# Kernel tuning notes

Measured on AMD Instinct MI355X. Metric: run time of the kernel, lower is better.

## Reference

```python
import jax, jax.numpy as jnp
import numpy as np

# Mistral-7B attention dims
B, S, D = 4, 1024, 4096
NH, NKV, HD = 32, 8, 128
SLIDING_WINDOW = 4096


def setup_inputs() -> dict:
    key = jax.random.key(0)
    ks = jax.random.split(key, 6)
    x = jax.random.normal(ks[0], (B, S, D), jnp.float32) * 0.02
    wq = jax.random.normal(ks[1], (NH * HD, D), jnp.float32) * 0.02
    wk = jax.random.normal(ks[2], (NKV * HD, D), jnp.float32) * 0.02
    wv = jax.random.normal(ks[3], (NKV * HD, D), jnp.float32) * 0.02
    wo = jax.random.normal(ks[4], (D, NH * HD), jnp.float32) * 0.02
    # RoPE frequencies (theta=10000), shape [S, HD//2]
    inv_freq = 1.0 / (10000.0 ** (jnp.arange(0, HD, 2, dtype=jnp.float32) / HD))
    angles = jnp.arange(S, dtype=jnp.float32)[:, None] * inv_freq[None, :]
    freqs_cos = jnp.cos(angles)
    freqs_sin = jnp.sin(angles)
    # sliding-window causal additive mask [S, S]
    i = jnp.arange(S)
    visible = (i[:, None] >= i[None, :]) & (i[:, None] - i[None, :] < SLIDING_WINDOW)
    mask = jnp.where(visible, 0.0, -1e9).astype(jnp.float32)
    positions = jnp.arange(S, dtype=jnp.int32)
    return {
        'x': x, 'wq': wq, 'wk': wk, 'wv': wv, 'wo': wo,
        'freqs_cos': freqs_cos, 'freqs_sin': freqs_sin,
        'mask': mask, 'positions': positions, 'seqlen': S,
    }


def _rope(t, fc, fs):
    # t: [B, S, H, HD]; fc/fs: [S, HD//2]; interleaved real/imag complex rotation
    tr = t[..., 0::2]
    ti = t[..., 1::2]
    fc = fc[None, :, None, :]
    fs = fs[None, :, None, :]
    out_r = tr * fc - ti * fs
    out_i = tr * fs + ti * fc
    return jnp.stack([out_r, out_i], axis=-1).reshape(t.shape)


def reference(x, wq, wk, wv, wo, freqs_cos, freqs_sin, mask, positions, seqlen):
    bsz = x.shape[0]
    scale = HD ** -0.5
    # QKV projections (TtLinear: y = x @ W^T, no bias)
    q = (x @ wq.T).reshape(bsz, seqlen, NH, HD)
    k = (x @ wk.T).reshape(bsz, seqlen, NKV, HD)
    v = (x @ wv.T).reshape(bsz, seqlen, NKV, HD)
    # inline rotary embedding on q, k
    q = _rope(q, freqs_cos, freqs_sin)
    k = _rope(k, freqs_cos, freqs_sin)
    # GQA: repeat_interleave kv heads (prefill path: positions.shape[0] > 1)
    rep = NH // NKV
    k = jnp.repeat(k, rep, axis=2)  # [B, S, NH, HD]
    v = jnp.repeat(v, rep, axis=2)
    scores = jnp.einsum('bqhd,bkhd->bhqk', q, k) * scale + mask[None, None]
    attn = jax.nn.softmax(scores, axis=-1)
    out = jnp.einsum('bhqk,bkhd->bqhd', attn, v).reshape(bsz, seqlen, NH * HD)
    return out @ wo.T
```

## Files before the change

kernel.cpp:

```cpp
#include <hip/hip_runtime.h>
#include <hip/hip_bf16.h>
#include <stdint.h>


typedef __bf16 bf16x8 __attribute__((ext_vector_type(8)));
typedef float floatx4 __attribute__((ext_vector_type(4)));

__device__ __forceinline__ unsigned short f2bf(float f) {
    union { float f; uint32_t u; } v; v.f = f;
    uint32_t u = v.u;
    uint32_t r = (u + 0x7FFFu + ((u >> 16) & 1u)) >> 16;
    return (unsigned short)r;
}
__device__ __forceinline__ float bf2f(unsigned short h) {
    union { uint32_t u; float f; } v; v.u = ((uint32_t)h) << 16;
    return v.f;
}

__device__ __forceinline__ void async_copy16(const void* g, void* l) {
    __builtin_amdgcn_global_load_lds(
        (const __attribute__((address_space(1))) unsigned int*)g,
        (__attribute__((address_space(3))) unsigned int*)l,
        16, 0, 0);
}

__global__ void cast_bf16_kernel(const float* __restrict__ in,
                                 unsigned short* __restrict__ out, int n4) {
    int i = blockIdx.x * blockDim.x + threadIdx.x;
    if (i >= n4) return;
    float4 v = ((const float4*)in)[i];
    ushort4 o;
    o.x = f2bf(v.x); o.y = f2bf(v.y); o.z = f2bf(v.z); o.w = f2bf(v.w);
    ((ushort4*)out)[i] = o;
}

#define GBM 128
#define GBN 128
#define GBK 64

__global__ __launch_bounds__(256)
void gemm_bt_kernel(const unsigned short* __restrict__ A,
                    const unsigned short* __restrict__ B,
                    void* __restrict__ Cout, int M, int N, int K, int out_is_bf16)
{
    __shared__ unsigned short As[GBM * GBK];
    __shared__ unsigned short Bs[GBN * GBK];

    const int tid  = threadIdx.x;
    const int lane = tid & 63;
    const int wave = tid >> 6;
    const int quad = lane >> 4;
    const int l15  = lane & 15;

    const int bm = blockIdx.y * GBM;
    const int bn = blockIdx.x * GBN;
    const int waveM = (wave >> 1) * 64;
    const int waveN = (wave & 1) * 64;

    floatx4 acc[4][4];
    #pragma unroll
    for (int i = 0; i < 4; i++)
        #pragma unroll
        for (int j = 0; j < 4; j++)
            acc[i][j] = floatx4{0.f, 0.f, 0.f, 0.f};

    const int srow = wave * 8 + (lane >> 3);
    const int gcol = (((lane & 7) ^ (lane >> 3)) << 4);
    uint8_t* AsB = (uint8_t*)As;
    uint8_t* BsB = (uint8_t*)Bs;

    for (int k0 = 0; k0 < K; k0 += GBK) {
        __syncthreads();
        const uint8_t* Ab = (const uint8_t*)A + (size_t)k0 * 2;
        const uint8_t* Bb = (const uint8_t*)B + (size_t)k0 * 2;
        #pragma unroll
        for (int i = 0; i < 4; i++) {
            int row = i * 32 + srow;
            async_copy16(Ab + (size_t)(bm + row) * K * 2 + gcol, AsB + i * 4096 + wave * 1024);
            async_copy16(Bb + (size_t)(bn + row) * K * 2 + gcol, BsB + i * 4096 + wave * 1024);
        }
        __syncthreads();

        #pragma unroll
        for (int kk = 0; kk < 2; kk++) {
            bf16x8 af[4], bfr[4];
            #pragma unroll
            for (int i = 0; i < 4; i++) {
                int row = waveM + i * 16 + l15;
                af[i] = *(const bf16x8*)(AsB + row * 128 +
                          ((((kk << 2) | quad) ^ (l15 & 7)) << 4));
            }
            #pragma unroll
            for (int j = 0; j < 4; j++) {
                int row = waveN + j * 16 + l15;
                bfr[j] = *(const bf16x8*)(BsB + row * 128 +
                          ((((kk << 2) | quad) ^ (l15 & 7)) << 4));
            }
            #pragma unroll
            for (int i = 0; i < 4; i++)
                #pragma unroll
                for (int j = 0; j < 4; j++)
                    acc[i][j] = __builtin_amdgcn_mfma_f32_16x16x32_bf16(af[i], bfr[j], acc[i][j], 0, 0, 0);
        }
    }

    const int rowBase = bm + waveM + quad * 4;
    const int colBase = bn + waveN + l15;
    if (out_is_bf16) {
        unsigned short* C = (unsigned short*)Cout;
        #pragma unroll
        for (int i = 0; i < 4; i++)
            #pragma unroll
            for (int j = 0; j < 4; j++)
                #pragma unroll
                for (int r = 0; r < 4; r++)
                    C[(size_t)(rowBase + i * 16 + r) * N + colBase + j * 16] = f2bf(acc[i][j][r]);
    } else {
        float* C = (float*)Cout;
        #pragma unroll
        for (int i = 0; i < 4; i++)
            #pragma unroll
            for (int j = 0; j < 4; j++)
                #pragma unroll
                for (int r = 0; r < 4; r++)
                    C[(size_t)(rowBase + i * 16 + r) * N + colBase + j * 16] = acc[i][j][r];
    }
}

__global__ __launch_bounds__(512, 2)
void gemm_bt_256_kernel(const unsigned short* __restrict__ A,
                        const unsigned short* __restrict__ B,
                        void* __restrict__ Cout, int M, int N, int K, int out_is_bf16)
{
    __shared__ uint8_t lds[4 * 32768];

    const int tid  = threadIdx.x;
    const int lane = tid & 63;
    const int wave = tid >> 6;
    const int quad = lane >> 4;
    const int l15  = lane & 15;
    const int wr   = wave >> 2;
    const int wc   = wave & 3;

    const int nwg = gridDim.x * gridDim.y;
    int orig = blockIdx.y * gridDim.x + blockIdx.x;
    int swzb = (nwg & 7) ? orig : ((orig & 7) * (nwg >> 3) + (orig >> 3));
    const int bm = (swzb / gridDim.x) * 256;
    const int bn = (swzb % gridDim.x) * 256;

    const int srow = wave * 32 + (lane >> 2);
    const int sg   = (((lane & 3) ^ ((lane >> 3) & 3)) << 4);
    const uint8_t* Ar0 = (const uint8_t*)(A + (size_t)(bm + srow) * K) + sg;
    const uint8_t* Ar1 = (const uint8_t*)(A + (size_t)(bm + srow + 16) * K) + sg;
    const uint8_t* Br0 = (const uint8_t*)(B + (size_t)(bn + srow) * K) + sg;
    const uint8_t* Br1 = (const uint8_t*)(B + (size_t)(bn + srow + 16) * K) + sg;
    const int ldsA0 = wave * 2048;
    const int ldsA1 = wave * 2048 + 1024;

    const int rsw  = (quad ^ ((l15 >> 1) & 3)) << 4;
    const int aoff = (wr * 128 + l15) * 64 + rsw;
    const int boff = 16384 + (wc * 64 + l15) * 64 + rsw;

    floatx4 acc[8][4];
    #pragma unroll
    for (int m = 0; m < 8; m++)
        #pragma unroll
        for (int n = 0; n < 4; n++)
            acc[m][n] = floatx4{0.f, 0.f, 0.f, 0.f};

    auto stage = [&](int t) {
        uint8_t* buf = lds + (size_t)(t & 3) * 32768;
        const size_t koff = (size_t)t * 64;
        async_copy16(Ar0 + koff, buf + ldsA0);
        async_copy16(Ar1 + koff, buf + ldsA1);
        async_copy16(Br0 + koff, buf + 16384 + ldsA0);
        async_copy16(Br1 + koff, buf + 16384 + ldsA1);
    };

    stage(0); stage(1); stage(2);

    const int NT = K >> 5;
    for (int t = 0; t < NT; ++t) {
        if (t < NT - 2)
            asm volatile("s_waitcnt vmcnt(8)\n\ts_barrier" ::: "memory");
        else if (t == NT - 2)
            asm volatile("s_waitcnt vmcnt(4)\n\ts_barrier" ::: "memory");
        else
            asm volatile("s_waitcnt vmcnt(0)\n\ts_barrier" ::: "memory");

        if (t + 3 < NT) stage(t + 3);

        const uint8_t* buf = lds + (size_t)(t & 3) * 32768;
        bf16x8 a0[4], b0[4], a1[4];
        #pragma unroll
        for (int m = 0; m < 4; m++) a0[m] = *(const bf16x8*)(buf + aoff + m * 1024);
        #pragma unroll
        for (int n = 0; n < 4; n++) b0[n] = *(const bf16x8*)(buf + boff + n * 1024);
        __builtin_amdgcn_s_setprio(1);
        #pragma unroll
        for (int m = 0; m < 4; m++)
            #pragma unroll
            for (int n = 0; n < 4; n++)
                acc[m][n] = __builtin_amdgcn_mfma_f32_16x16x32_bf16(a0[m], b0[n], acc[m][n], 0, 0, 0);
        __builtin_amdgcn_s_setprio(0);
        #pragma unroll
        for (int m = 0; m < 4; m++) a1[m] = *(const bf16x8*)(buf + aoff + (4 + m) * 1024);
        __builtin_amdgcn_s_setprio(1);
        #pragma unroll
        for (int m = 0; m < 4; m++)
            #pragma unroll
            for (int n = 0; n < 4; n++)
                acc[4 + m][n] = __builtin_amdgcn_mfma_f32_16x16x32_bf16(a1[m], b0[n], acc[4 + m][n], 0, 0, 0);
        __builtin_amdgcn_s_setprio(0);
    }

    const int rowBase = bm + wr * 128 + quad * 4;
    const int colBase = bn + wc * 64 + l15;
    if (out_is_bf16) {
        unsigned short* C = (unsigned short*)Cout;
        #pragma unroll
        for (int m = 0; m < 8; m++)
            #pragma unroll
            for (int n = 0; n < 4; n++)
                #pragma unroll
                for (int r = 0; r < 4; r++)
                    C[(size_t)(rowBase + m * 16 + r) * N + colBase + n * 16] = f2bf(acc[m][n][r]);
    } else {
        float* C = (float*)Cout;
        #pragma unroll
        for (int m = 0; m < 8; m++)
            #pragma unroll
            for (int n = 0; n < 4; n++)
                #pragma unroll
                for (int r = 0; r < 4; r++)
                    C[(size_t)(rowBase + m * 16 + r) * N + colBase + n * 16] = acc[m][n][r];
    }
}

__global__ void rope_kernel(unsigned short* __restrict__ t,
                            const float* __restrict__ fc,
                            const float* __restrict__ fs,
                            int nh, int total_pairs) {
    int idx = blockIdx.x * blockDim.x + threadIdx.x;
    if (idx >= total_pairs) return;
    int j   = idx & 63;
    int tmp = idx >> 6;
    int s   = (tmp / nh) & 1023;
    float c  = fc[s * 64 + j];
    float sn = fs[s * 64 + j];
    size_t base = (size_t)tmp * 128 + j * 2;
    float tr = bf2f(t[base]), ti = bf2f(t[base + 1]);
    t[base]     = f2bf(tr * c - ti * sn);
    t[base + 1] = f2bf(tr * sn + ti * c);
}

#define AS_  1024
#define AHD 128
#define ANH 32
#define ANKV 8

__global__ __launch_bounds__(256)
void attn_kernel(const unsigned short* __restrict__ Q,
                 const unsigned short* __restrict__ Kk,
                 const unsigned short* __restrict__ Vt,
                 unsigned short* __restrict__ O)
{
    __shared__ unsigned short Ks[64 * 136];
    __shared__ unsigned short Vs[128 * 72];
    __shared__ unsigned short Ps[4][16 * 72];

    const int tid  = threadIdx.x;
    const int lane = tid & 63;
    const int wave = tid >> 6;
    const int quad = lane >> 4;
    const int l15  = lane & 15;

    const int bid = blockIdx.x;
    const int qt = 15 - (bid & 15);
    const int h  = (bid >> 4) & 31;
    const int b  = bid >> 9;
    const int hk = h >> 2;
    const int q0 = qt * 64;

    bf16x8 aq[4];
    {
        const int qrow = q0 + wave * 16 + l15;
        const unsigned short* src = Q + ((size_t)((b * AS_ + qrow) * ANH + h)) * AHD;
        #pragma unroll
        for (int kk = 0; kk < 4; kk++)
            aq[kk] = *(const bf16x8*)(src + kk * 32 + quad * 8);
    }

    float lsum[4];
    #pragma unroll
    for (int r = 0; r < 4; r++) lsum[r] = 0.0f;
    floatx4 o[8];
    #pragma unroll
    for (int d = 0; d < 8; d++) o[d] = floatx4{0.f, 0.f, 0.f, 0.f};

    const float scale = 0.08838834764831845f;

    for (int kt = 0; kt <= qt; kt++) {
        __syncthreads();
        #pragma unroll
        for (int i = 0; i < 4; i++) {
            int c = tid + i * 256;
            int r = c >> 4, col = (c & 15) * 8;
            size_t krow = ((size_t)((b * AS_ + kt * 64 + r) * ANKV + hk)) * AHD;
            *(uint4*)(Ks + r * 136 + col) = *(const uint4*)(Kk + krow + col);
        }
        #pragma unroll
        for (int i = 0; i < 4; i++) {
            int c = tid + i * 256;
            int d = c >> 3, kk0 = (c & 7) * 8;
            const unsigned short* src =
                Vt + (size_t)(hk * AHD + d) * (4 * AS_) + b * AS_ + kt * 64 + kk0;
            *(uint4*)(Vs + d * 72 + kk0) = *(const uint4*)src;
        }
        __syncthreads();

        floatx4 sc[4];
        #pragma unroll
        for (int j = 0; j < 4; j++) {
            sc[j] = floatx4{0.f, 0.f, 0.f, 0.f};
            #pragma unroll
            for (int kk = 0; kk < 4; kk++) {
                bf16x8 bk = *(const bf16x8*)(Ks + (j * 16 + l15) * 136 + kk * 32 + quad * 8);
                sc[j] = __builtin_amdgcn_mfma_f32_16x16x32_bf16(aq[kk], bk, sc[j], 0, 0, 0);
            }
        }

        const bool diag = (kt == qt);
        #pragma unroll
        for (int r = 0; r < 4; r++) {
            const int qrow = q0 + wave * 16 + quad * 4 + r;
            float acc = 0.0f;
            #pragma unroll
            for (int j = 0; j < 4; j++) {
                float e = __expf(sc[j][r] * scale);
                if (diag) {
                    int key = kt * 64 + j * 16 + l15;
                    if (key > qrow) e = 0.0f;
                }
                acc += e;
                Ps[wave][(quad * 4 + r) * 72 + j * 16 + l15] = f2bf(e);
            }
            lsum[r] += acc;
        }

        #pragma unroll
        for (int kk = 0; kk < 2; kk++) {
            bf16x8 ap = *(const bf16x8*)(Ps[wave] + l15 * 72 + kk * 32 + quad * 8);
            #pragma unroll
            for (int d = 0; d < 8; d++) {
                bf16x8 bv = *(const bf16x8*)(Vs + (d * 16 + l15) * 72 + kk * 32 + quad * 8);
                o[d] = __builtin_amdgcn_mfma_f32_16x16x32_bf16(ap, bv, o[d], 0, 0, 0);
            }
        }
    }

    #pragma unroll
    for (int r = 0; r < 4; r++) {
        float s = lsum[r];
        #pragma unroll
        for (int off = 1; off < 16; off <<= 1)
            s += __shfl_xor(s, off, 64);
        float inv = 1.0f / s;
        int qrow = q0 + wave * 16 + quad * 4 + r;
        unsigned short* dst = O + ((size_t)((b * AS_ + qrow) * ANH + h)) * AHD;
        #pragma unroll
        for (int d = 0; d < 8; d++)
            dst[d * 16 + l15] = f2bf(o[d][r] * inv);
    }
}

extern "C" void kernel_launch(void* const* d_in, const int* in_sizes, int n_in,
                              void* d_out, int out_size, void* d_ws, size_t ws_size,
                              hipStream_t stream)
{
    const float* x  = (const float*)d_in[0];
    const float* wq = (const float*)d_in[1];
    const float* wk = (const float*)d_in[2];
    const float* wv = (const float*)d_in[3];
    const float* wo = (const float*)d_in[4];
    const float* fc = (const float*)d_in[5];
    const float* fs = (const float*)d_in[6];

    const int B = 4, S = 1024, D = 4096, NH = 32, NKV = 8, HD = 128;
    const int M    = B * S;
    const int NQ   = NH * HD;
    const int NKVD = NKV * HD;

    unsigned short* ws = (unsigned short*)d_ws;
    size_t off = 0;
    unsigned short* xb  = ws + off; off += (size_t)M * D;
    unsigned short* wqb = ws + off; off += (size_t)NQ * D;
    unsigned short* wkb = ws + off; off += (size_t)NKVD * D;
    unsigned short* wvb = ws + off; off += (size_t)NKVD * D;
    unsigned short* wob = ws + off; off += (size_t)D * NQ;
    unsigned short* qb  = ws + off; off += (size_t)M * NQ;
    unsigned short* kb  = ws + off; off += (size_t)M * NKVD;
    unsigned short* vtb = ws + off; off += (size_t)NKVD * M;
    unsigned short* aob = ws + off; off += (size_t)M * NQ;

    {
        struct { const float* src; unsigned short* dst; size_t n; } jobs[5] = {
            { x,  xb,  (size_t)M * D },
            { wq, wqb, (size_t)NQ * D },
            { wk, wkb, (size_t)NKVD * D },
            { wv, wvb, (size_t)NKVD * D },
            { wo, wob, (size_t)D * NQ },
        };
        for (int i = 0; i < 5; i++) {
            int n4 = (int)(jobs[i].n / 4);
            cast_bf16_kernel<<<(n4 + 255) / 256, 256, 0, stream>>>(jobs[i].src, jobs[i].dst, n4);
        }
    }

    gemm_bt_256_kernel<<<dim3(NQ / 256,  M / 256), 512, 0, stream>>>(xb,  wqb, qb,  M,   NQ, D, 1);
    gemm_bt_kernel<<<dim3(NKVD / GBN, M / GBM), 256, 0, stream>>>(xb,  wkb, kb,  M, NKVD, D, 1);
    gemm_bt_kernel<<<dim3(M / GBN, NKVD / GBM), 256, 0, stream>>>(wvb, xb,  vtb, NKVD, M, D, 1);

    {
        int pq = M * NH * (HD / 2);
        rope_kernel<<<(pq + 255) / 256, 256, 0, stream>>>(qb, fc, fs, NH, pq);
        int pk = M * NKV * (HD / 2);
        rope_kernel<<<(pk + 255) / 256, 256, 0, stream>>>(kb, fc, fs, NKV, pk);
    }

    attn_kernel<<<B * NH * (S / 64), 256, 0, stream>>>(qb, kb, vtb, aob);

    gemm_bt_256_kernel<<<dim3(D / 256, M / 256), 512, 0, stream>>>(aob, wob, d_out, M, D, NQ, 0);
}
```

Before: 852.2 us.

## Restructure attention kernel with 128-row query tiles and async double-buffered K/V

```diff
diff --git a/kernel.cpp b/kernel.cpp
--- a/kernel.cpp
+++ b/kernel.cpp
@@ -259,15 +259,13 @@
 #define ANH 32
 #define ANKV 8
 
-__global__ __launch_bounds__(256)
+__global__ __launch_bounds__(512, 4)
 void attn_kernel(const unsigned short* __restrict__ Q,
                  const unsigned short* __restrict__ Kk,
                  const unsigned short* __restrict__ Vt,
                  unsigned short* __restrict__ O)
 {
-    __shared__ unsigned short Ks[64 * 136];
-    __shared__ unsigned short Vs[128 * 72];
-    __shared__ unsigned short Ps[4][16 * 72];
+    __shared__ uint8_t lds[81920];
 
     const int tid  = threadIdx.x;
     const int lane = tid & 63;
@@ -276,16 +274,41 @@
     const int l15  = lane & 15;
 
     const int bid = blockIdx.x;
-    const int qt = 15 - (bid & 15);
-    const int h  = (bid >> 4) & 31;
-    const int b  = bid >> 9;
-    const int hk = h >> 2;
-    const int q0 = qt * 64;
+    const int qt2 = 7 - (bid & 7);
+    const int h   = (bid >> 3) & 31;
+    const int b   = bid >> 8;
+    const int hk  = h >> 2;
+    const int q0  = qt2 * 128;
+
+    uint8_t* ldsK = lds;
+    uint8_t* ldsV = lds + 32768;
+    uint8_t* Ps   = lds + 65536 + wave * 2048;
+
+    const int krow0 = (2 * wave + 0) * 4 + (lane >> 4);
+    const int krow1 = (2 * wave + 1) * 4 + (lane >> 4);
+    const int kg0 = ((lane & 15) ^ (0 + (lane >> 4))) * 8;
+    const int kg1 = ((lane & 15) ^ (4 + (lane >> 4))) * 8;
+    const unsigned short* Kg0 = Kk + ((size_t)(b * AS_ + krow0) * ANKV + hk) * AHD + kg0;
+    const unsigned short* Kg1 = Kk + ((size_t)(b * AS_ + krow1) * ANKV + hk) * AHD + kg1;
+    const int vrow0 = (2 * wave + 0) * 8 + (lane >> 3);
+    const int vrow1 = (2 * wave + 1) * 8 + (lane >> 3);
+    const int vg = ((lane & 7) ^ (lane >> 3)) * 8;
+    const unsigned short* Vg0 = Vt + (size_t)(hk * AHD + vrow0) * (4 * AS_) + b * AS_ + vg;
+    const unsigned short* Vg1 = Vt + (size_t)(hk * AHD + vrow1) * (4 * AS_) + b * AS_ + vg;
+
+    auto stage = [&](int t) {
+        uint8_t* kb_ = ldsK + (t & 1) * 16384;
+        uint8_t* vb_ = ldsV + (t & 1) * 16384;
+        async_copy16(Kg0 + (size_t)t * 65536, kb_ + (2 * wave + 0) * 1024);
+        async_copy16(Kg1 + (size_t)t * 65536, kb_ + (2 * wave + 1) * 1024);
+        async_copy16(Vg0 + t * 64, vb_ + (2 * wave + 0) * 1024);
+        async_copy16(Vg1 + t * 64, vb_ + (2 * wave + 1) * 1024);
+    };
 
     bf16x8 aq[4];
     {
         const int qrow = q0 + wave * 16 + l15;
-        const unsigned short* src = Q + ((size_t)((b * AS_ + qrow) * ANH + h)) * AHD;
+        const unsigned short* src = Q + ((size_t)(b * AS_ + qrow) * ANH + h) * AHD;
         #pragma unroll
         for (int kk = 0; kk < 4; kk++)
             aq[kk] = *(const bf16x8*)(src + kk * 32 + quad * 8);
@@ -299,64 +322,74 @@
     for (int d = 0; d < 8; d++) o[d] = floatx4{0.f, 0.f, 0.f, 0.f};
 
     const float scale = 0.08838834764831845f;
-
-    for (int kt = 0; kt <= qt; kt++) {
-        __syncthreads();
-        #pragma unroll
-        for (int i = 0; i < 4; i++) {
-            int c = tid + i * 256;
-            int r = c >> 4, col = (c & 15) * 8;
-            size_t krow = ((size_t)((b * AS_ + kt * 64 + r) * ANKV + hk)) * AHD;
-            *(uint4*)(Ks + r * 136 + col) = *(const uint4*)(Kk + krow + col);
+    const int wMaxKt = (q0 + wave * 16 + 15) >> 6;
+    const int ktMax  = (q0 + 127) >> 6;
+
+    stage(0);
+    const int swz = (l15 & 7) << 4;
+
+    for (int kt = 0; kt <= ktMax; ++kt) {
+        if (kt < ktMax) {
+            stage(kt + 1);
+            asm volatile("s_waitcnt vmcnt(4)\n\ts_barrier" ::: "memory");
+        } else {
+            asm volatile("s_waitcnt vmcnt(0)\n\ts_barrier" ::: "memory");
         }
-        #pragma unroll
-        for (int i = 0; i < 4; i++) {
-            int c = tid + i * 256;
-            int d = c >> 3, kk0 = (c & 7) * 8;
-            const unsigned short* src =
-                Vt + (size_t)(hk * AHD + d) * (4 * AS_) + b * AS_ + kt * 64 + kk0;
-            *(uint4*)(Vs + d * 72 + kk0) = *(const uint4*)src;
+
+        if (kt <= wMaxKt) {
+            const uint8_t* kb_ = ldsK + (kt & 1) * 16384;
+            const uint8_t* vb_ = ldsV + (kt & 1) * 16384;
+
+            floatx4 sc[4];
+            #pragma unroll
+            for (int j = 0; j < 4; j++) sc[j] = floatx4{0.f, 0.f, 0.f, 0.f};
+            __builtin_amdgcn_s_setprio(1);
+            #pragma unroll
+            for (int j = 0; j < 4; j++)
+                #pragma unroll
+                for (int kk = 0; kk < 4; kk++) {
+                    bf16x8 bk = *(const bf16x8*)(kb_ + (j * 16 + l15) * 256 +
+                                  (((kk * 4 + quad) << 4) ^ swz));
+                    sc[j] = __builtin_amdgcn_mfma_f32_16x16x32_bf16(aq[kk], bk, sc[j], 0, 0, 0);
+                }
+            __builtin_amdgcn_s_setprio(0);
+
+            #pragma unroll
+            for (int r = 0; r < 4; r++) {
+                const int row  = quad * 4 + r;
+                const int qrow = q0 + wave * 16 + row;
+                const bool needMask = (kt * 64 + 63 > qrow);
+                float acc = 0.0f;
+                #pragma unroll
+                for (int j = 0; j < 4; j++) {
+                    float e = __expf(sc[j][r] * scale);
+                    if (needMask) {
+                        int key = kt * 64 + j * 16 + l15;
+                        if (key > qrow) e = 0.0f;
+                    }
+                    acc += e;
+                    int g = (j * 2 + (l15 >> 3)) ^ (row & 7);
+                    *(unsigned short*)(Ps + row * 128 + (g << 4) + (l15 & 7) * 2) = f2bf(e);
+                }
+                lsum[r] += acc;
+            }
+
+            __builtin_amdgcn_s_setprio(1);
+            #pragma unroll
+            for (int kk = 0; kk < 2; kk++) {
+                bf16x8 ap = *(const bf16x8*)(Ps + l15 * 128 +
+                              (((kk * 4 + quad) << 4) ^ swz));
+                #pragma unroll
+                for (int d = 0; d < 8; d++) {
+                    bf16x8 bv = *(const bf16x8*)(vb_ + (d * 16 + l15) * 128 +
+                                  (((kk * 4 + quad) << 4) ^ swz));
+                    o[d] = __builtin_amdgcn_mfma_f32_16x16x32_bf16(ap, bv, o[d], 0, 0, 0);
+                }
+            }
+            __builtin_amdgcn_s_setprio(0);
         }
-        __syncthreads();
-
-        floatx4 sc[4];
-        #pragma unroll
-        for (int j = 0; j < 4; j++) {
-            sc[j] = floatx4{0.f, 0.f, 0.f, 0.f};
-            #pragma unroll
-            for (int kk = 0; kk < 4; kk++) {
-                bf16x8 bk = *(const bf16x8*)(Ks + (j * 16 + l15) * 136 + kk * 32 + quad * 8);
-                sc[j] = __builtin_amdgcn_mfma_f32_16x16x32_bf16(aq[kk], bk, sc[j], 0, 0, 0);
-            }
-        }
-
-        const bool diag = (kt == qt);
-        #pragma unroll
-        for (int r = 0; r < 4; r++) {
-            const int qrow = q0 + wave * 16 + quad * 4 + r;
-            float acc = 0.0f;
-            #pragma unroll
-            for (int j = 0; j < 4; j++) {
-                float e = __expf(sc[j][r] * scale);
-                if (diag) {
-                    int key = kt * 64 + j * 16 + l15;
-                    if (key > qrow) e = 0.0f;
-                }
-                acc += e;
-                Ps[wave][(quad * 4 + r) * 72 + j * 16 + l15] = f2bf(e);
-            }
-            lsum[r] += acc;
-        }
-
-        #pragma unroll
-        for (int kk = 0; kk < 2; kk++) {
-            bf16x8 ap = *(const bf16x8*)(Ps[wave] + l15 * 72 + kk * 32 + quad * 8);
-            #pragma unroll
-            for (int d = 0; d < 8; d++) {
-                bf16x8 bv = *(const bf16x8*)(Vs + (d * 16 + l15) * 72 + kk * 32 + quad * 8);
-                o[d] = __builtin_amdgcn_mfma_f32_16x16x32_bf16(ap, bv, o[d], 0, 0, 0);
-            }
-        }
+
+        asm volatile("s_barrier" ::: "memory");
     }
 
     #pragma unroll
@@ -367,7 +400,7 @@
             s += __shfl_xor(s, off, 64);
         float inv = 1.0f / s;
         int qrow = q0 + wave * 16 + quad * 4 + r;
-        unsigned short* dst = O + ((size_t)((b * AS_ + qrow) * ANH + h)) * AHD;
+        unsigned short* dst = O + ((size_t)(b * AS_ + qrow) * ANH + h) * AHD;
         #pragma unroll
         for (int d = 0; d < 8; d++)
             dst[d * 16 + l15] = f2bf(o[d][r] * inv);
@@ -428,7 +461,7 @@
         rope_kernel<<<(pk + 255) / 256, 256, 0, stream>>>(kb, fc, fs, NKV, pk);
     }
 
-    attn_kernel<<<B * NH * (S / 64), 256, 0, stream>>>(qb, kb, vtb, aob);
+    attn_kernel<<<B * NH * (S / 128), 512, 0, stream>>>(qb, kb, vtb, aob);
 
     gemm_bt_256_kernel<<<dim3(D / 256, M / 256), 512, 0, stream>>>(aob, wob, d_out, M, D, NQ, 0);
 }
```

Result: faster. 741.3 us (-13.0%).
